# Kernel tuning notes

Hardware: AMD Instinct MI355X
Metric: run time of the kernel (lower is better)

Reference implementation:

```python
import jax, jax.numpy as jnp
import numpy as np

KERNEL_SIZE = 9
STRIDE = 1
LN_EPS = 1e-5


def _toeplitz(L, dtype):
    # T[t, l] = 1 iff l - t == STRIDE * i for i in range(KERNEL_SIZE // STRIDE)
    d = jnp.arange(L)[None, :] - jnp.arange(L)[:, None]
    mask = (d >= 0) & (d % STRIDE == 0) & ((d // STRIDE) < (KERNEL_SIZE // STRIDE))
    return mask.astype(dtype)


def setup_inputs() -> dict:
    key = jax.random.key(0)
    ks = jax.random.split(key, 4)
    N, Cin, L, V = 16, 256, 300, 25
    P, Cout = 3, 256
    x = jax.random.normal(ks[0], (N, Cin, L, V), dtype=jnp.float32)
    A = jax.random.uniform(ks[1], (P, V, V), dtype=jnp.float32)
    conv_w = jax.random.normal(ks[2], (Cout * P, Cin), dtype=jnp.float32) * 0.02
    conv_b = jax.random.normal(ks[3], (Cout * P,), dtype=jnp.float32) * 0.02
    ln_gamma = jnp.ones((Cout, 1, V), dtype=jnp.float32)
    ln_beta = jnp.zeros((Cout, 1, V), dtype=jnp.float32)
    edge_importance = jnp.ones((P, V * V), dtype=jnp.float32)
    return {"x": x, "A": A, "conv_w": conv_w, "conv_b": conv_b,
            "ln_gamma": ln_gamma, "ln_beta": ln_beta,
            "edge_importance": edge_importance}


def reference(x, A, conv_w, conv_b, ln_gamma, ln_beta, edge_importance):
    N, Cin, L, V = x.shape
    P = A.shape[0]
    Cout = conv_w.shape[0] // P

    res = x  # in_channels == out_channels and stride == 1 -> identity residual

    # 1x1 conv -> (N, Cout*P, L, V); split into P chunks of Cout along channels
    y = jnp.einsum('nclv,oc->nolv', x, conv_w) + conv_b[None, :, None, None]
    y = y.reshape(N, P, Cout, L, V)  # chunk p == channels [p*Cout:(p+1)*Cout]

    # partitioned graph aggregation with edge importance: (P,V,V) adjacency
    Aw = A * edge_importance.reshape(P, V, V)
    y = jnp.einsum('npclv,pvw->npclw', y, Aw)  # (N, P, Cout, L, V)

    # temporal conv via toeplitz matmul over frame dim L
    T = _toeplitz(L, y.dtype)
    y = jnp.einsum('npclv,lm->npcmv', y, T)  # (N, P, Cout, L, V)

    # sum over partitions -> (N, Cout, L, V)
    y = y.sum(axis=1)

    # LayerNorm over (C, V) per (n, l), affine params shaped (Cout, 1, V)
    mu = jnp.mean(y, axis=(1, 3), keepdims=True)
    var = jnp.var(y, axis=(1, 3), keepdims=True)
    y = (y - mu) * jax.lax.rsqrt(var + LN_EPS)
    y = y * ln_gamma[None] + ln_beta[None]
    y = jax.nn.relu(y)

    # residual add, final ReLU (dropout rate 0.0 -> identity)
    return jax.nn.relu(y + res)
```

## Files before the change

### kernel.cpp

```cpp
#include <hip/hip_runtime.h>

#define NN 16
#define CIN 256
#define COUT 256
#define LL 300
#define VV 25
#define PP 3
#define KS 9
#define KK 768
#define MM (NN*LL*VV)
#define MPAD 120064
#define MBLK 938

typedef float floatx4 __attribute__((ext_vector_type(4)));
typedef short short8 __attribute__((ext_vector_type(8)));

__device__ __forceinline__ unsigned short f2bf(float f) {
    unsigned u = __builtin_bit_cast(unsigned, f);
    u += 0x7fff + ((u >> 16) & 1);
    return (unsigned short)(u >> 16);
}
__device__ __forceinline__ float bf2f(unsigned short h) {
    unsigned u = ((unsigned)h) << 16;
    return __builtin_bit_cast(float, u);
}
__device__ __forceinline__ void gl2lds16(const void* g, void* l) {
    __builtin_amdgcn_global_load_lds(
        (const __attribute__((address_space(1))) void*)g,
        (__attribute__((address_space(3))) void*)l, 16, 0, 0);
}

__global__ __launch_bounds__(256) void k_prep(
    const float* __restrict__ A, const float* __restrict__ conv_w,
    const float* __restrict__ conv_b, const float* __restrict__ ei,
    unsigned short* __restrict__ w2t, float* __restrict__ bias2,
    unsigned short* __restrict__ xa)
{
    const int t = blockIdx.x * 256 + threadIdx.x;
    const int nthr = gridDim.x * 256;
    for (int idx = t; idx < COUT * KK; idx += nthr) {
        int c = idx / KK, k = idx % KK, p = k >> 8, ci = k & 255;
        w2t[idx] = f2bf(conv_w[(p * COUT + c) * CIN + ci]);
    }
    for (int idx = t; idx < COUT * VV; idx += nthr) {
        int c = idx / VV, w = idx % VV;
        float s = 0.f;
        for (int p = 0; p < PP; ++p) {
            float cs = 0.f;
            for (int v = 0; v < VV; ++v) {
                int a = (p * VV + v) * VV + w;
                cs += A[a] * ei[a];
            }
            s += conv_b[p * COUT + c] * cs;
        }
        bias2[idx] = s;
    }
    for (int idx = t; idx < (MPAD - MM) * KK; idx += nthr)
        xa[(size_t)MM * KK + idx] = 0;
}

__global__ __launch_bounds__(256) void k_agg(
    const float* __restrict__ x, const float* __restrict__ A,
    const float* __restrict__ ei, unsigned short* __restrict__ xa)
{
    __shared__ float Aw[PP * VV * VV];
    const int l = blockIdx.x, n = blockIdx.y, t = threadIdx.x;
    for (int idx = t; idx < PP * VV * VV; idx += 256)
        Aw[idx] = A[idx] * ei[idx];
    __syncthreads();

    float xv[VV];
    const float* xp = x + ((size_t)(n * CIN + t) * LL + l) * VV;
    #pragma unroll
    for (int v = 0; v < VV; ++v) xv[v] = xp[v];

    const size_t mrow = (size_t)(n * LL + l) * VV;
    #pragma unroll
    for (int p = 0; p < PP; ++p) {
        float acc[VV];
        #pragma unroll
        for (int w = 0; w < VV; ++w) acc[w] = 0.f;
        #pragma unroll
        for (int v = 0; v < VV; ++v) {
            const float xvv = xv[v];
            const float* ar = &Aw[(p * VV + v) * VV];
            #pragma unroll
            for (int w = 0; w < VV; ++w) acc[w] += xvv * ar[w];
        }
        #pragma unroll
        for (int w = 0; w < VV; ++w)
            xa[(mrow + w) * KK + p * CIN + t] = f2bf(acc[w]);
    }
}

__global__ __launch_bounds__(256) void k_gemm(
    const unsigned short* __restrict__ xa,
    const unsigned short* __restrict__ w2t,
    unsigned short* __restrict__ z)
{
    __shared__ __align__(16) unsigned short As[128 * 32];
    __shared__ __align__(16) unsigned short Bs[128 * 32];
    const int t = threadIdx.x, wv = t >> 6, ln = t & 63;
    const int m0 = blockIdx.x * 128, c0 = blockIdx.y * 128;

    floatx4 acc[4][4];
    #pragma unroll
    for (int i = 0; i < 4; ++i)
        #pragma unroll
        for (int j = 0; j < 4; ++j)
            acc[i][j] = (floatx4){0.f, 0.f, 0.f, 0.f};

    const int srow = wv * 32 + (ln >> 2);
    const int scol = (ln & 3) * 8;
    const int mw = (wv >> 1) * 64, nw = (wv & 1) * 64;
    const int frow = ln & 15, fcol = (ln >> 4) * 8;

    for (int kt = 0; kt < KK / 32; ++kt) {
        const int k0 = kt * 32;
        __syncthreads();
        gl2lds16(xa  + (size_t)(m0 + srow)      * KK + k0 + scol, &As[(wv * 32) * 32]);
        gl2lds16(xa  + (size_t)(m0 + srow + 16) * KK + k0 + scol, &As[(wv * 32 + 16) * 32]);
        gl2lds16(w2t + (size_t)(c0 + srow)      * KK + k0 + scol, &Bs[(wv * 32) * 32]);
        gl2lds16(w2t + (size_t)(c0 + srow + 16) * KK + k0 + scol, &Bs[(wv * 32 + 16) * 32]);
        __syncthreads();

        short8 af[4], bf[4];
        #pragma unroll
        for (int i = 0; i < 4; ++i)
            af[i] = *(const short8*)&As[(mw + i * 16 + frow) * 32 + fcol];
        #pragma unroll
        for (int j = 0; j < 4; ++j)
            bf[j] = *(const short8*)&Bs[(nw + j * 16 + frow) * 32 + fcol];
        #pragma unroll
        for (int i = 0; i < 4; ++i)
            #pragma unroll
            for (int j = 0; j < 4; ++j)
                acc[i][j] = __builtin_amdgcn_mfma_f32_16x16x32_bf16(af[j] * 0 + af[i], bf[j], acc[i][j], 0, 0, 0);
    }

    const int q = ln >> 4, cL = ln & 15;
    #pragma unroll
    for (int i = 0; i < 4; ++i) {
        #pragma unroll
        for (int j = 0; j < 4; ++j) {
            #pragma unroll
            for (int r = 0; r < 4; ++r) {
                const int m = m0 + mw + i * 16 + q * 4 + r;
                const int c = c0 + nw + j * 16 + cL;
                if (m < MM) z[(size_t)m * COUT + c] = f2bf(acc[i][j][r]);
            }
        }
    }
}

__global__ __launch_bounds__(256) void k_ln(
    const unsigned short* __restrict__ z, const float* __restrict__ x,
    const float* __restrict__ bias2, const float* __restrict__ gamma,
    const float* __restrict__ beta, float* __restrict__ out)
{
    const int m = blockIdx.x, n = blockIdx.y, t = threadIdx.x;
    float zw[VV];
    #pragma unroll
    for (int w = 0; w < VV; ++w) zw[w] = 0.f;

    const int l0 = (m >= KS - 1) ? (m - (KS - 1)) : 0;
    for (int l = l0; l <= m; ++l) {
        const unsigned short* zp = z + (size_t)((n * LL + l) * VV) * COUT + t;
        #pragma unroll
        for (int w = 0; w < VV; ++w) zw[w] += bf2f(zp[(size_t)w * COUT]);
    }
    const float cnt = (float)(m - l0 + 1);
    const float* b2 = bias2 + t * VV;
    #pragma unroll
    for (int w = 0; w < VV; ++w) zw[w] += cnt * b2[w];

    float s1 = 0.f, s2 = 0.f;
    #pragma unroll
    for (int w = 0; w < VV; ++w) { s1 += zw[w]; s2 += zw[w] * zw[w]; }

    __shared__ float rs[4], rq[4], stats[2];
    #pragma unroll
    for (int off = 32; off; off >>= 1) { s1 += __shfl_down(s1, off); s2 += __shfl_down(s2, off); }
    const int wid = t >> 6, lane = t & 63;
    if (lane == 0) { rs[wid] = s1; rq[wid] = s2; }
    __syncthreads();
    if (t == 0) {
        const float S1 = rs[0] + rs[1] + rs[2] + rs[3];
        const float S2 = rq[0] + rq[1] + rq[2] + rq[3];
        const float inv = 1.f / (COUT * VV);
        const float mu = S1 * inv;
        const float var = S2 * inv - mu * mu;
        stats[0] = mu;
        stats[1] = rsqrtf(var + 1e-5f);
    }
    __syncthreads();
    const float mu = stats[0], rsd = stats[1];

    const float* gp = gamma + t * VV;
    const float* bp = beta + t * VV;
    const float* xp = x + ((size_t)(n * CIN + t) * LL + m) * VV;
    float* op = out + ((size_t)(n * COUT + t) * LL + m) * VV;
    #pragma unroll
    for (int w = 0; w < VV; ++w) {
        float val = (zw[w] - mu) * rsd * gp[w] + bp[w];
        val = fmaxf(val, 0.f);
        val += xp[w];
        op[w] = fmaxf(val, 0.f);
    }
}

extern "C" void kernel_launch(void* const* d_in, const int* in_sizes, int n_in,
                              void* d_out, int out_size, void* d_ws, size_t ws_size,
                              hipStream_t stream) {
    const float* x      = (const float*)d_in[0];
    const float* A      = (const float*)d_in[1];
    const float* conv_w = (const float*)d_in[2];
    const float* conv_b = (const float*)d_in[3];
    const float* gamma  = (const float*)d_in[4];
    const float* beta   = (const float*)d_in[5];
    const float* ei     = (const float*)d_in[6];
    float* out = (float*)d_out;

    char* ws = (char*)d_ws;
    unsigned short* xa  = (unsigned short*)ws;
    unsigned short* z   = (unsigned short*)(ws + 184418304);
    unsigned short* w2t = (unsigned short*)(ws + 245891072);
    float*          b2  = (float*)(ws + 246284288);

    k_prep<<<64, 256, 0, stream>>>(A, conv_w, conv_b, ei, w2t, b2, xa);
    k_agg<<<dim3(LL, NN), 256, 0, stream>>>(x, A, ei, xa);
    k_gemm<<<dim3(MBLK, 2), 256, 0, stream>>>(xa, w2t, z);
    k_ln<<<dim3(LL, NN), 256, 0, stream>>>(z, x, b2, gamma, beta, out);
}
```

Baseline: 592.4 us.

## Move temporal window sum before graph aggregation using sliding window over x

```diff
diff --git a/kernel.cpp b/kernel.cpp
--- a/kernel.cpp
+++ b/kernel.cpp
@@ -5,12 +5,14 @@
 #define COUT 256
 #define LL 300
 #define VV 25
+#define VP 28
 #define PP 3
 #define KS 9
 #define KK 768
 #define MM (NN*LL*VV)
 #define MPAD 120064
 #define MBLK 938
+#define TM 10
 
 typedef float floatx4 __attribute__((ext_vector_type(4)));
 typedef short short8 __attribute__((ext_vector_type(8)));
@@ -59,37 +61,65 @@
         xa[(size_t)MM * KK + idx] = 0;
 }
 
-__global__ __launch_bounds__(256) void k_agg(
+__global__ __launch_bounds__(256) void k1_temporal_agg(
     const float* __restrict__ x, const float* __restrict__ A,
     const float* __restrict__ ei, unsigned short* __restrict__ xa)
 {
-    __shared__ float Aw[PP * VV * VV];
-    const int l = blockIdx.x, n = blockIdx.y, t = threadIdx.x;
-    for (int idx = t; idx < PP * VV * VV; idx += 256)
-        Aw[idx] = A[idx] * ei[idx];
+    __shared__ float AwL[PP * VV * VP];
+    const int n = blockIdx.y, t = threadIdx.x;
+    const int m0 = blockIdx.x * TM;
+
+    for (int idx = t; idx < PP * VV * VV; idx += 256) {
+        int pv = idx / VV, w = idx % VV;
+        AwL[pv * VP + w] = A[idx] * ei[idx];
+    }
     __syncthreads();
 
-    float xv[VV];
-    const float* xp = x + ((size_t)(n * CIN + t) * LL + l) * VV;
-    #pragma unroll
-    for (int v = 0; v < VV; ++v) xv[v] = xp[v];
-
-    const size_t mrow = (size_t)(n * LL + l) * VV;
-    #pragma unroll
-    for (int p = 0; p < PP; ++p) {
-        float acc[VV];
-        #pragma unroll
-        for (int w = 0; w < VV; ++w) acc[w] = 0.f;
-        #pragma unroll
-        for (int v = 0; v < VV; ++v) {
-            const float xvv = xv[v];
-            const float* ar = &Aw[(p * VV + v) * VV];
-            #pragma unroll
-            for (int w = 0; w < VV; ++w) acc[w] += xvv * ar[w];
-        }
-        #pragma unroll
-        for (int w = 0; w < VV; ++w)
-            xa[(mrow + w) * KK + p * CIN + t] = f2bf(acc[w]);
+    const float* xbase = x + (size_t)(n * CIN + t) * LL * VV;
+
+    float wsum[VV];
+    #pragma unroll
+    for (int v = 0; v < VV; ++v) wsum[v] = 0.f;
+    const int lw0 = (m0 >= KS - 1) ? (m0 - (KS - 1)) : 0;
+    for (int l = lw0; l <= m0; ++l) {
+        const float* xp = xbase + l * VV;
+        #pragma unroll
+        for (int v = 0; v < VV; ++v) wsum[v] += xp[v];
+    }
+
+    for (int m = m0; m < m0 + TM; ++m) {
+        if (m > m0) {
+            const float* xp = xbase + m * VV;
+            #pragma unroll
+            for (int v = 0; v < VV; ++v) wsum[v] += xp[v];
+            if (m - KS >= 0) {
+                const float* xo = xbase + (m - KS) * VV;
+                #pragma unroll
+                for (int v = 0; v < VV; ++v) wsum[v] -= xo[v];
+            }
+        }
+        const size_t mrow = (size_t)(n * LL + m) * VV;
+        #pragma unroll
+        for (int p = 0; p < PP; ++p) {
+            float acc[VV];
+            #pragma unroll
+            for (int w = 0; w < VV; ++w) acc[w] = 0.f;
+            #pragma unroll
+            for (int v = 0; v < VV; ++v) {
+                const float xvv = wsum[v];
+                const float* ar = &AwL[(p * VV + v) * VP];
+                #pragma unroll
+                for (int wq = 0; wq < 24; wq += 4) {
+                    const float4 f = *(const float4*)(ar + wq);
+                    acc[wq + 0] += xvv * f.x; acc[wq + 1] += xvv * f.y;
+                    acc[wq + 2] += xvv * f.z; acc[wq + 3] += xvv * f.w;
+                }
+                acc[24] += xvv * ar[24];
+            }
+            #pragma unroll
+            for (int w = 0; w < VV; ++w)
+                xa[(mrow + w) * KK + p * CIN + t] = f2bf(acc[w]);
+        }
     }
 }
 
@@ -135,7 +165,7 @@
         for (int i = 0; i < 4; ++i)
             #pragma unroll
             for (int j = 0; j < 4; ++j)
-                acc[i][j] = __builtin_amdgcn_mfma_f32_16x16x32_bf16(af[j] * 0 + af[i], bf[j], acc[i][j], 0, 0, 0);
+                acc[i][j] = __builtin_amdgcn_mfma_f32_16x16x32_bf16(af[i], bf[j], acc[i][j], 0, 0, 0);
     }
 
     const int q = ln >> 4, cL = ln & 15;
@@ -159,20 +189,15 @@
     const float* __restrict__ beta, float* __restrict__ out)
 {
     const int m = blockIdx.x, n = blockIdx.y, t = threadIdx.x;
+    const int l0 = (m >= KS - 1) ? (m - (KS - 1)) : 0;
+    const float cnt = (float)(m - l0 + 1);
+
     float zw[VV];
-    #pragma unroll
-    for (int w = 0; w < VV; ++w) zw[w] = 0.f;
-
-    const int l0 = (m >= KS - 1) ? (m - (KS - 1)) : 0;
-    for (int l = l0; l <= m; ++l) {
-        const unsigned short* zp = z + (size_t)((n * LL + l) * VV) * COUT + t;
-        #pragma unroll
-        for (int w = 0; w < VV; ++w) zw[w] += bf2f(zp[(size_t)w * COUT]);
-    }
-    const float cnt = (float)(m - l0 + 1);
+    const unsigned short* zp = z + (size_t)((n * LL + m) * VV) * COUT + t;
     const float* b2 = bias2 + t * VV;
     #pragma unroll
-    for (int w = 0; w < VV; ++w) zw[w] += cnt * b2[w];
+    for (int w = 0; w < VV; ++w)
+        zw[w] = bf2f(zp[(size_t)w * COUT]) + cnt * b2[w];
 
     float s1 = 0.f, s2 = 0.f;
     #pragma unroll
@@ -228,7 +253,7 @@
     float*          b2  = (float*)(ws + 246284288);
 
     k_prep<<<64, 256, 0, stream>>>(A, conv_w, conv_b, ei, w2t, b2, xa);
-    k_agg<<<dim3(LL, NN), 256, 0, stream>>>(x, A, ei, xa);
+    k1_temporal_agg<<<dim3(LL / TM, NN), 256, 0, stream>>>(x, A, ei, xa);
     k_gemm<<<dim3(MBLK, 2), 256, 0, stream>>>(xa, w2t, z);
     k_ln<<<dim3(LL, NN), 256, 0, stream>>>(z, x, b2, gamma, beta, out);
 }
```

After: 802.2 us. +35.4%, slower.
